# Performance work log

Hardware: AMD Instinct MI355X
Metric: run time of the kernel (lower is better)

## Reference

```python
import jax, jax.numpy as jnp
import numpy as np

B, L, K, H, D = 2, 512, 128, 32, 1024
NUM_EDGES = 2048
SQRT_2PI = 2.5066282746310002
MIN_F32 = float(np.finfo(np.float32).min)
SCALING = K ** -0.5


def setup_inputs() -> dict:
    key = jax.random.key(0)
    ks = jax.random.split(key, 18)
    pos = jax.random.normal(ks[0], (B, L, 3), jnp.float32) * 10.0
    node_type_edge = jax.random.randint(ks[1], (B, L, L, 2), 0, NUM_EDGES)
    adj = jax.random.randint(ks[2], (B, L, L), 0, 2).astype(bool)
    # last 64 tokens of second sample are padding
    padding_mask = jnp.arange(L)[None, :] >= jnp.array([L, L - 64])[:, None]
    molecule_mask = jax.random.randint(ks[3], (B, L), 0, 2).astype(bool)
    clean_mask = jax.random.randint(ks[4], (B, L), 0, 2).astype(bool)
    # parameters
    pos_emb_w = jax.random.normal(ks[5], (K, 3), jnp.float32) * 0.1            # nn.Linear(3, K, bias=False)
    pos_feature_emb_w = jax.random.normal(ks[6], (D, K), jnp.float32) * (K ** -0.5)  # nn.Linear(K, D, bias=False)
    gbf_means = jax.random.uniform(ks[7], (K,), jnp.float32, minval=0.0, maxval=3.0)
    gbf_stds = jax.random.uniform(ks[8], (K,), jnp.float32, minval=0.1, maxval=3.0)
    gbf_mul = jax.random.normal(ks[9], (NUM_EDGES, 1), jnp.float32) * 0.1 + 1.0
    gbf_bias = jax.random.normal(ks[10], (NUM_EDGES, 1), jnp.float32) * 0.1
    proj_w1 = jax.random.normal(ks[11], (K, K), jnp.float32) * (K ** -0.5)     # NonLinear layer1
    proj_b1 = jnp.zeros((K,), jnp.float32)
    proj_w2 = jax.random.normal(ks[12], (H, K), jnp.float32) * (K ** -0.5)     # NonLinear layer2
    proj_b2 = jnp.zeros((H,), jnp.float32)
    pos_proj_w = jax.random.normal(ks[13], (D, K), jnp.float32) * (K ** -0.5)  # pos_embedding_proj
    pos_proj_b = jnp.zeros((D,), jnp.float32)
    return dict(pos=pos, node_type_edge=node_type_edge, adj=adj, padding_mask=padding_mask,
                molecule_mask=molecule_mask, clean_mask=clean_mask,
                pos_emb_w=pos_emb_w, pos_feature_emb_w=pos_feature_emb_w,
                gbf_means=gbf_means, gbf_stds=gbf_stds, gbf_mul=gbf_mul, gbf_bias=gbf_bias,
                proj_w1=proj_w1, proj_b1=proj_b1, proj_w2=proj_w2, proj_b2=proj_b2,
                pos_proj_w=pos_proj_w, pos_proj_b=pos_proj_b)


def reference(pos, node_type_edge, adj, padding_mask, molecule_mask, clean_mask,
              pos_emb_w, pos_feature_emb_w, gbf_means, gbf_stds, gbf_mul, gbf_bias,
              proj_w1, proj_b1, proj_w2, proj_b2, pos_proj_w, pos_proj_b):
    # pairwise distances [B,L,L] (eps-safe sqrt; grad at diagonal is 0)
    delta = pos[:, :, None, :] - pos[:, None, :, :]
    dist0 = jnp.sqrt(jnp.sum(delta * delta, axis=-1) + 1e-12)

    # adj forced True on non-molecule / clean rows
    adj = jnp.where(~molecule_mask[:, :, None], True, adj)
    adj = jnp.where(clean_mask[:, :, None], True, adj)

    # GaussianLayer: per-edge-type affine on dist, then K gaussian kernels -> [B,L,L,K]
    mul = gbf_mul[node_type_edge].sum(axis=-2)    # [B,L,L,1]
    bia = gbf_bias[node_type_edge].sum(axis=-2)   # [B,L,L,1]
    x = mul * dist0[..., None] + bia              # [B,L,L,1]
    std = jnp.abs(gbf_stds) + 1e-5                # [K]
    edge_feature = jnp.exp(-0.5 * jnp.square((x - gbf_means) / std)) / (SQRT_2PI * std)  # [B,L,L,K]

    # NonLinear projection to heads
    h = jax.nn.gelu(jnp.einsum('blmk,jk->blmj', edge_feature, proj_w1) + proj_b1, approximate=False)
    gab = jnp.einsum('blmj,nj->blmn', h, proj_w2) + proj_b2   # [B,L,L,H]

    expand_mask = padding_mask
    gab = jnp.where(expand_mask[:, None, :, None], -jnp.inf, gab)
    gab = jnp.where(~adj[..., None], -jnp.inf, gab)
    gab = jnp.where(padding_mask[:, :, None, None], 0.0, gab)
    graph_attn_bias = jnp.transpose(gab, (0, 3, 1, 2))        # [B,H,L,L]

    dist = graph_attn_bias.sum(axis=1)                        # [B,L,L]
    dist = jnp.where(expand_mask[:, None, :], MIN_F32, dist)
    dist = jnp.where(padding_mask[:, :, None], MIN_F32, dist)

    pos_emb = jnp.einsum('blc,kc->blk', pos, pos_emb_w)       # [B,L,K]
    pos_emb = jnp.where(expand_mask[..., None], 0.0, pos_emb)

    dist = jnp.where(~adj, MIN_F32, dist)
    dist = jax.nn.softmax(dist.astype(jnp.float32) * SCALING, axis=-1)

    pfe = jnp.einsum('blm,bmk->blk', dist, pos_emb)           # weighted aggregation
    pfe = jnp.einsum('blk,dk->bld', pfe, pos_feature_emb_w)   # Linear(K, D, bias=False)

    ef = jnp.where(expand_mask[:, None, :, None], 0.0, edge_feature).sum(axis=-2)  # [B,L,K]
    pfe = pfe + jnp.einsum('blk,dk->bld', ef, pos_proj_w) + pos_proj_b
    pfe = jnp.where(padding_mask[..., None], 0.0, pfe)
    return pfe, graph_attn_bias
```

## Files before the change

### kernel.cpp

```cpp
#include <hip/hip_runtime.h>

typedef __attribute__((ext_vector_type(8))) short short8;
typedef __attribute__((ext_vector_type(4))) float f32x4;

static const int BB = 2;
static const int LL = 512;
#define MIN_F32 (-3.4028234663852886e+38f)
#define NEG_BIG (-1.0e38f)
#define SCALING_F 0.08838834764831845f
#define SQ2PI 2.5066282746310002f

__device__ __forceinline__ float gelu_fast(float x) {
    float s  = x * 0.70710678118654752440f;
    float za = fabsf(s);
    float t  = __builtin_amdgcn_rcpf(fmaf(za, 0.3275911f, 1.0f));
    float p  = t * fmaf(t, fmaf(t, fmaf(t, fmaf(t, 1.061405429f, -1.453152027f),
                                        1.421413741f), -0.284496736f), 0.254829592f);
    float e  = __expf(-za * za);
    float q  = fmaf(-p, e, 1.0f);
    union { float f; unsigned u; } uq, us;
    uq.f = q; us.f = s;
    uq.u = (uq.u & 0x7FFFFFFFu) | (us.u & 0x80000000u);
    float hx = 0.5f * x;
    return fmaf(hx, uq.f, hx);
}
__device__ __forceinline__ unsigned short f2bf(float f) {
    union { float f; unsigned int u; } v; v.f = f;
    unsigned int u = v.u;
    return (unsigned short)((u + 0x7FFFu + ((u >> 16) & 1u)) >> 16);
}
__device__ __forceinline__ int swz(int row, int bytecol) {
    return row * 256 + (bytecol ^ ((row & 7) << 4));
}

__global__ __launch_bounds__(256) void prep_kernel(
    const float* __restrict__ wfe, const float* __restrict__ wp,
    float* __restrict__ wfet, float* __restrict__ wpt)
{
    int idx = blockIdx.x * 256 + threadIdx.x;
    int which = idx >> 17;
    int r = idx & 131071;
    int k = r >> 10;
    int d = r & 1023;
    if (which == 0) wfet[r] = wfe[d * 128 + k];
    else            wpt[r]  = wp[d * 128 + k];
}

__global__ __launch_bounds__(512, 4) void row_kernel(
    const float* __restrict__ pos,
    const int*   __restrict__ nte,
    const unsigned char* __restrict__ adj,
    const unsigned char* __restrict__ padm,
    const unsigned char* __restrict__ molm,
    const unsigned char* __restrict__ clnm,
    const float* __restrict__ gmean,
    const float* __restrict__ gstd,
    const float* __restrict__ gmul,
    const float* __restrict__ gbias,
    const float* __restrict__ w1,
    const float* __restrict__ b1,
    const float* __restrict__ w2,
    const float* __restrict__ b2,
    const float* __restrict__ pw,
    float* __restrict__ out_gab,
    float* __restrict__ pfe1,
    float* __restrict__ efsum)
{
    __shared__ __align__(16) char W1s[128 * 256];
    __shared__ __align__(16) char W2s[32 * 256];
    __shared__ __align__(16) char efs[64 * 256];
    __shared__ __align__(16) char hs [64 * 256];
    __shared__ float dist_row[512];
    __shared__ float xval[512];
    __shared__ unsigned char flgall[512];
    __shared__ float b1s[128];
    __shared__ float b2s[32];
    __shared__ float sred[16];
    __shared__ float dsump[128];

    const int t = threadIdx.x;
    const int row = blockIdx.x;
    const int b = row >> 9;
    const int i = row & 511;

    const int w  = t >> 6;
    const int l  = t & 63;
    const int lr = l & 15;
    const int lq = l >> 4;

    for (int idx = t; idx < 2048 + 512; idx += 512) {
        const float* src; char* dst; int r16, c16;
        if (idx < 2048) { r16 = idx >> 4;          c16 = idx & 15; src = w1 + r16 * 128 + c16 * 8; dst = W1s; }
        else            { r16 = (idx - 2048) >> 4; c16 = (idx - 2048) & 15; src = w2 + r16 * 128 + c16 * 8; dst = W2s; }
        float4 f0 = *(const float4*)(src);
        float4 f1 = *(const float4*)(src + 4);
        uint4 pk;
        pk.x = (unsigned)f2bf(f0.x) | ((unsigned)f2bf(f0.y) << 16);
        pk.y = (unsigned)f2bf(f0.z) | ((unsigned)f2bf(f0.w) << 16);
        pk.z = (unsigned)f2bf(f1.x) | ((unsigned)f2bf(f1.y) << 16);
        pk.w = (unsigned)f2bf(f1.z) | ((unsigned)f2bf(f1.w) << 16);
        *(uint4*)(dst + swz(r16, c16 * 16)) = pk;
    }
    if (t < 128) b1s[t] = b1[t];
    if (t < 32)  b2s[t] = b2[t];

    const bool pad_i = padm[row] != 0;
    const bool force_adj = (clnm[row] != 0) || (molm[row] == 0);
    const float pix = pos[row * 3 + 0], piy = pos[row * 3 + 1], piz = pos[row * 3 + 2];

    {
        int2 e2 = ((const int2*)nte)[row * 512 + t];
        float mul = gmul[e2.x] + gmul[e2.y];
        float bia = gbias[e2.x] + gbias[e2.y];
        float dx = pix - pos[(b * 512 + t) * 3 + 0];
        float dy = piy - pos[(b * 512 + t) * 3 + 1];
        float dz = piz - pos[(b * 512 + t) * 3 + 2];
        float dist = sqrtf(dx * dx + dy * dy + dz * dz + 1e-12f);
        xval[t] = mul * dist + bia;
        int padj = padm[b * 512 + t] ? 1 : 0;
        int adje = (force_adj || adj[row * 512 + t]) ? 2 : 0;
        flgall[t] = (unsigned char)(padj | adje);
    }

    const int kk = t & 127;
    const float gs = fabsf(gstd[kk]) + 1e-5f;
    const float mean_r = gmean[kk];
    const float istd_r = 1.0f / gs;
    const float lnc = -logf(SQ2PI * gs);
    float efacc = 0.f;

    __syncthreads();

    for (int tile = 0; tile < 8; ++tile) {
        const int j0 = tile * 64;
        if (tile > 0 && t < 64) {
            int fl = flgall[j0 - 64 + t];
            bool masked = pad_i || (fl & 1) || !(fl & 2);
            dist_row[j0 - 64 + t] = masked ? MIN_F32 : (dsump[t] + dsump[64 + t]);
        }
        {
            const int jg0 = j0 + (t >> 7) * 16;
            #pragma unroll
            for (int jj = 0; jj < 16; ++jj) {
                int j = jg0 + jj;
                float x = xval[j];
                float mk = (flgall[j] & 1) ? 0.0f : 1.0f;
                float a = (x - mean_r) * istd_r;
                float e = __expf(fmaf(a * a, -0.5f, lnc));
                *(unsigned short*)(efs + swz((j & 63), 2 * kk)) = f2bf(e);
                efacc = fmaf(e, mk, efacc);
            }
        }
        __syncthreads();
        {
            const int jr = (w & 1) * 32;
            const int jc = (w >> 1) * 32;
            f32x4 a00 = {0.f,0.f,0.f,0.f}, a01 = a00, a10 = a00, a11 = a00;
            #pragma unroll
            for (int ks = 0; ks < 4; ++ks) {
                int bcol = ks * 64 + lq * 16;
                short8 av0 = *(const short8*)(efs + swz(jr + lr, bcol));
                short8 av1 = *(const short8*)(efs + swz(jr + 16 + lr, bcol));
                short8 bv0 = *(const short8*)(W1s + swz(jc + lr, bcol));
                short8 bv1 = *(const short8*)(W1s + swz(jc + 16 + lr, bcol));
                a00 = __builtin_amdgcn_mfma_f32_16x16x32_bf16(av0, bv0, a00, 0, 0, 0);
                a01 = __builtin_amdgcn_mfma_f32_16x16x32_bf16(av0, bv1, a01, 0, 0, 0);
                a10 = __builtin_amdgcn_mfma_f32_16x16x32_bf16(av1, bv0, a10, 0, 0, 0);
                a11 = __builtin_amdgcn_mfma_f32_16x16x32_bf16(av1, bv1, a11, 0, 0, 0);
            }
            #pragma unroll
            for (int mi = 0; mi < 2; ++mi) {
                #pragma unroll
                for (int ci = 0; ci < 2; ++ci) {
                    f32x4 acc = (mi == 0) ? (ci == 0 ? a00 : a01) : (ci == 0 ? a10 : a11);
                    int jo = jc + ci * 16 + lr;
                    float bb = b1s[jo];
                    #pragma unroll
                    for (int r = 0; r < 4; ++r) {
                        int j = jr + mi * 16 + lq * 4 + r;
                        *(unsigned short*)(hs + swz(j, 2 * jo)) = f2bf(gelu_fast(acc[r] + bb));
                    }
                }
            }
        }
        __syncthreads();
        {
            const int mt = w >> 2;
            const int jt2 = w & 3;
            f32x4 acc = (f32x4){0.f, 0.f, 0.f, 0.f};
            #pragma unroll
            for (int ks = 0; ks < 4; ++ks) {
                int bcol = ks * 64 + lq * 16;
                short8 av = *(const short8*)(W2s + swz(mt * 16 + lr, bcol));
                short8 bv = *(const short8*)(hs + swz(jt2 * 16 + lr, bcol));
                acc = __builtin_amdgcn_mfma_f32_16x16x32_bf16(av, bv, acc, 0, 0, 0);
            }
            int jl = jt2 * 16 + lr;
            int jg = j0 + jl;
            int fl = flgall[jg];
            bool kill = (fl & 1) || !(fl & 2);
            float dpart = 0.f;
            size_t base = ((size_t)(b * 32 + mt * 16 + lq * 4) * 512 + i) * 512 + jg;
            #pragma unroll
            for (int r = 0; r < 4; ++r) {
                float raw = acc[r] + b2s[mt * 16 + lq * 4 + r];
                dpart += raw;
                float outv = pad_i ? 0.0f : (kill ? NEG_BIG : raw);
                out_gab[base + (size_t)r * 262144] = outv;
            }
            dpart += __shfl_xor(dpart, 16);
            dpart += __shfl_xor(dpart, 32);
            if (l < 16) dsump[mt * 64 + jl] = dpart;
        }
        __syncthreads();
    }

    float* rb = (float*)efs;
    if (t < 64) {
        int fl = flgall[448 + t];
        bool masked = pad_i || (fl & 1) || !(fl & 2);
        dist_row[448 + t] = masked ? MIN_F32 : (dsump[t] + dsump[64 + t]);
    }
    rb[t] = efacc;
    __syncthreads();
    if (t < 128) {
        efsum[(size_t)row * 128 + t] = rb[t] + rb[128 + t] + rb[256 + t] + rb[384 + t];
    }

    float sv = dist_row[t] * SCALING_F;
    float v = sv;
    #pragma unroll
    for (int m = 32; m > 0; m >>= 1) v = fmaxf(v, __shfl_xor(v, m));
    if ((t & 63) == 0) sred[t >> 6] = v;
    __syncthreads();
    float mx = sred[0];
    #pragma unroll
    for (int w8 = 1; w8 < 8; ++w8) mx = fmaxf(mx, sred[w8]);
    float e = expf(sv - mx);
    v = e;
    #pragma unroll
    for (int m = 32; m > 0; m >>= 1) v += __shfl_xor(v, m);
    if ((t & 63) == 0) sred[8 + (t >> 6)] = v;
    __syncthreads();
    float sm = 0.f;
    #pragma unroll
    for (int w8 = 0; w8 < 8; ++w8) sm += sred[8 + w8];
    float p = e / sm;

    float px = pos[(b * 512 + t) * 3 + 0];
    float py = pos[(b * 512 + t) * 3 + 1];
    float pz = pos[(b * 512 + t) * 3 + 2];
    float vx = p * px, vy = p * py, vz = p * pz;
    #pragma unroll
    for (int m = 32; m > 0; m >>= 1) {
        vx += __shfl_xor(vx, m); vy += __shfl_xor(vy, m); vz += __shfl_xor(vz, m);
    }
    __syncthreads();
    if ((t & 63) == 0) {
        int w8 = t >> 6;
        rb[w8] = vx; rb[8 + w8] = vy; rb[16 + w8] = vz;
    }
    __syncthreads();
    if (t < 128) {
        float w0 = 0.f, w1v = 0.f, w2v = 0.f;
        #pragma unroll
        for (int w8 = 0; w8 < 8; ++w8) {
            w0 += rb[w8]; w1v += rb[8 + w8]; w2v += rb[16 + w8];
        }
        pfe1[(size_t)row * 128 + t] = pw[t * 3 + 0] * w0 + pw[t * 3 + 1] * w1v + pw[t * 3 + 2] * w2v;
    }
}

__global__ __launch_bounds__(256) void pfe_kernel(
    const float* __restrict__ pfe1,
    const float* __restrict__ efsum,
    const float* __restrict__ wfet,
    const float* __restrict__ wpt,
    const float* __restrict__ pb,
    const unsigned char* __restrict__ padm,
    float* __restrict__ out)
{
    __shared__ __align__(16) float As[2 * 32 * 132];
    __shared__ __align__(16) float Bs[2 * 16 * 128];
    const int t  = threadIdx.x;
    const int tx = t & 31;
    const int ty = t >> 5;
    const int r0 = (blockIdx.x >> 3) * 32;
    const int d0 = (blockIdx.x & 7) * 128;

    #pragma unroll
    for (int q = 0; q < 16; ++q) {
        int ii = t + q * 256;
        int r = ii >> 7, k = ii & 127;
        As[(0 * 32 + r) * 132 + k] = pfe1 [(size_t)(r0 + r) * 128 + k];
        As[(1 * 32 + r) * 132 + k] = efsum[(size_t)(r0 + r) * 128 + k];
    }

    f32x4 acc[4];
    #pragma unroll
    for (int rr = 0; rr < 4; ++rr) acc[rr] = (f32x4){0.f, 0.f, 0.f, 0.f};

    for (int kc = 0; kc < 8; ++kc) {
        __syncthreads();
        #pragma unroll
        for (int q = 0; q < 2; ++q) {
            int ii = t + q * 256;
            int kr = ii >> 5, dq = ii & 31;
            f32x4 v0 = ((const f32x4*)(wfet + (size_t)(kc * 16 + kr) * 1024 + d0))[dq];
            f32x4 v1 = ((const f32x4*)(wpt  + (size_t)(kc * 16 + kr) * 1024 + d0))[dq];
            *(f32x4*)&Bs[(0 * 16 + kr) * 128 + dq * 4] = v0;
            *(f32x4*)&Bs[(1 * 16 + kr) * 128 + dq * 4] = v1;
        }
        __syncthreads();
        #pragma unroll
        for (int k4 = 0; k4 < 4; ++k4) {
            int kb = kc * 16 + k4 * 4;
            f32x4 a0[4], a1[4];
            #pragma unroll
            for (int rr = 0; rr < 4; ++rr) {
                int r = ty * 4 + rr;
                a0[rr] = *(const f32x4*)&As[(0 * 32 + r) * 132 + kb];
                a1[rr] = *(const f32x4*)&As[(1 * 32 + r) * 132 + kb];
            }
            #pragma unroll
            for (int kq = 0; kq < 4; ++kq) {
                f32x4 b0 = *(const f32x4*)&Bs[(0 * 16 + k4 * 4 + kq) * 128 + tx * 4];
                f32x4 b1 = *(const f32x4*)&Bs[(1 * 16 + k4 * 4 + kq) * 128 + tx * 4];
                #pragma unroll
                for (int rr = 0; rr < 4; ++rr) {
                    acc[rr] += a0[rr][kq] * b0 + a1[rr][kq] * b1;
                }
            }
        }
    }

    f32x4 bv = *(const f32x4*)&pb[d0 + tx * 4];
    #pragma unroll
    for (int rr = 0; rr < 4; ++rr) {
        int row = r0 + ty * 4 + rr;
        f32x4 o = acc[rr] + bv;
        if (padm[row]) o = (f32x4){0.f, 0.f, 0.f, 0.f};
        *(f32x4*)&out[(size_t)row * 1024 + d0 + tx * 4] = o;
    }
}

extern "C" void kernel_launch(void* const* d_in, const int* in_sizes, int n_in,
                              void* d_out, int out_size, void* d_ws, size_t ws_size,
                              hipStream_t stream) {
    const float* pos  = (const float*)d_in[0];
    const int*   nte  = (const int*)d_in[1];
    const unsigned char* adj  = (const unsigned char*)d_in[2];
    const unsigned char* padm = (const unsigned char*)d_in[3];
    const unsigned char* molm = (const unsigned char*)d_in[4];
    const unsigned char* clnm = (const unsigned char*)d_in[5];
    const float* pw    = (const float*)d_in[6];
    const float* wfe   = (const float*)d_in[7];
    const float* gmean = (const float*)d_in[8];
    const float* gstd  = (const float*)d_in[9];
    const float* gmul  = (const float*)d_in[10];
    const float* gbias = (const float*)d_in[11];
    const float* w1    = (const float*)d_in[12];
    const float* b1    = (const float*)d_in[13];
    const float* w2    = (const float*)d_in[14];
    const float* b2    = (const float*)d_in[15];
    const float* wp    = (const float*)d_in[16];
    const float* pb    = (const float*)d_in[17];

    float* out      = (float*)d_out;
    float* out_pfe  = out;
    float* out_gab  = out + (size_t)BB * LL * 1024;

    float* ws    = (float*)d_ws;
    float* pfe1  = ws;
    float* efsum = ws + 131072;
    float* wfet  = ws + 262144;
    float* wpt   = ws + 393216;

    prep_kernel<<<1024, 256, 0, stream>>>(wfe, wp, wfet, wpt);
    row_kernel<<<BB * LL, 512, 0, stream>>>(pos, nte, adj, padm, molm, clnm,
                                            gmean, gstd, gmul, gbias,
                                            w1, b1, w2, b2, pw,
                                            out_gab, pfe1, efsum);
    pfe_kernel<<<256, 256, 0, stream>>>(pfe1, efsum, wfet, wpt, pb, padm, out_pfe);
}
```

Before: 117.3 us.

## Vectorize Gaussian-basis and GELU LDS writes via thread remap and MFMA operand swap

Each thread now computes 8 consecutive Gaussian basis channels for 2 edge positions and writes them to shared memory as one packed 16-byte store, replacing 16 scattered 2-byte stores. The first MFMA now takes the weight as the A operand and the basis tile as the B operand. This transposes the accumulator layout, so GELU outputs go out as packed bf16x2 8-byte stores and the bias comes in as a float4. The per-channel edge-feature sum reduction is reworked to match, now summing 32 partials per channel instead of 4. The cost is more registers held for per-channel constants and accumulators, and a longer final reduction.

```diff
diff --git a/kernel.cpp b/kernel.cpp
--- a/kernel.cpp
+++ b/kernel.cpp
@@ -1,4 +1,5 @@
 #include <hip/hip_runtime.h>
+#include <hip/hip_bf16.h>
 
 typedef __attribute__((ext_vector_type(8))) short short8;
 typedef __attribute__((ext_vector_type(4))) float f32x4;
@@ -23,6 +24,11 @@
     uq.u = (uq.u & 0x7FFFFFFFu) | (us.u & 0x80000000u);
     float hx = 0.5f * x;
     return fmaf(hx, uq.f, hx);
+}
+__device__ __forceinline__ unsigned pack_bf16x2(float lo, float hi) {
+    __hip_bfloat162 h2 = __float22bfloat162_rn(float2{lo, hi});
+    union { __hip_bfloat162 h; unsigned u; } v; v.h = h2;
+    return v.u;
 }
 __device__ __forceinline__ unsigned short f2bf(float f) {
     union { float f; unsigned int u; } v; v.f = f;
@@ -122,12 +128,17 @@
         flgall[t] = (unsigned char)(padj | adje);
     }
 
-    const int kk = t & 127;
-    const float gs = fabsf(gstd[kk]) + 1e-5f;
-    const float mean_r = gmean[kk];
-    const float istd_r = 1.0f / gs;
-    const float lnc = -logf(SQ2PI * gs);
-    float efacc = 0.f;
+    const int k0 = (t & 15) * 8;
+    const int js = t >> 4;
+    float mean_q[8], istd_q[8], lnc_q[8], efacc[8];
+    #pragma unroll
+    for (int q = 0; q < 8; ++q) {
+        float gsv = fabsf(gstd[k0 + q]) + 1e-5f;
+        mean_q[q] = gmean[k0 + q];
+        istd_q[q] = 1.0f / gsv;
+        lnc_q[q]  = -logf(SQ2PI * gsv);
+        efacc[q]  = 0.f;
+    }
 
     __syncthreads();
 
@@ -138,31 +149,36 @@
             bool masked = pad_i || (fl & 1) || !(fl & 2);
             dist_row[j0 - 64 + t] = masked ? MIN_F32 : (dsump[t] + dsump[64 + t]);
         }
-        {
-            const int jg0 = j0 + (t >> 7) * 16;
-            #pragma unroll
-            for (int jj = 0; jj < 16; ++jj) {
-                int j = jg0 + jj;
-                float x = xval[j];
-                float mk = (flgall[j] & 1) ? 0.0f : 1.0f;
-                float a = (x - mean_r) * istd_r;
-                float e = __expf(fmaf(a * a, -0.5f, lnc));
-                *(unsigned short*)(efs + swz((j & 63), 2 * kk)) = f2bf(e);
-                efacc = fmaf(e, mk, efacc);
-            }
+        #pragma unroll
+        for (int jj = 0; jj < 2; ++jj) {
+            int j = js + jj * 32;
+            float x  = xval[j0 + j];
+            float mk = (flgall[j0 + j] & 1) ? 0.0f : 1.0f;
+            unsigned pk[4];
+            #pragma unroll
+            for (int q = 0; q < 4; ++q) {
+                float a0 = (x - mean_q[2*q+0]) * istd_q[2*q+0];
+                float a1 = (x - mean_q[2*q+1]) * istd_q[2*q+1];
+                float e0 = __expf(fmaf(a0 * a0, -0.5f, lnc_q[2*q+0]));
+                float e1 = __expf(fmaf(a1 * a1, -0.5f, lnc_q[2*q+1]));
+                efacc[2*q+0] = fmaf(e0, mk, efacc[2*q+0]);
+                efacc[2*q+1] = fmaf(e1, mk, efacc[2*q+1]);
+                pk[q] = pack_bf16x2(e0, e1);
+            }
+            *(uint4*)(efs + swz(j, 2 * k0)) = make_uint4(pk[0], pk[1], pk[2], pk[3]);
         }
         __syncthreads();
         {
-            const int jr = (w & 1) * 32;
-            const int jc = (w >> 1) * 32;
+            const int jobase = (w & 3) * 32;
+            const int jbase  = (w >> 2) * 32;
             f32x4 a00 = {0.f,0.f,0.f,0.f}, a01 = a00, a10 = a00, a11 = a00;
             #pragma unroll
             for (int ks = 0; ks < 4; ++ks) {
                 int bcol = ks * 64 + lq * 16;
-                short8 av0 = *(const short8*)(efs + swz(jr + lr, bcol));
-                short8 av1 = *(const short8*)(efs + swz(jr + 16 + lr, bcol));
-                short8 bv0 = *(const short8*)(W1s + swz(jc + lr, bcol));
-                short8 bv1 = *(const short8*)(W1s + swz(jc + 16 + lr, bcol));
+                short8 av0 = *(const short8*)(W1s + swz(jobase + lr, bcol));
+                short8 av1 = *(const short8*)(W1s + swz(jobase + 16 + lr, bcol));
+                short8 bv0 = *(const short8*)(efs + swz(jbase + lr, bcol));
+                short8 bv1 = *(const short8*)(efs + swz(jbase + 16 + lr, bcol));
                 a00 = __builtin_amdgcn_mfma_f32_16x16x32_bf16(av0, bv0, a00, 0, 0, 0);
                 a01 = __builtin_amdgcn_mfma_f32_16x16x32_bf16(av0, bv1, a01, 0, 0, 0);
                 a10 = __builtin_amdgcn_mfma_f32_16x16x32_bf16(av1, bv0, a10, 0, 0, 0);
@@ -170,16 +186,18 @@
             }
             #pragma unroll
             for (int mi = 0; mi < 2; ++mi) {
+                int jo0 = jobase + mi * 16 + lq * 4;
+                float4 bb = *(const float4*)&b1s[jo0];
                 #pragma unroll
                 for (int ci = 0; ci < 2; ++ci) {
                     f32x4 acc = (mi == 0) ? (ci == 0 ? a00 : a01) : (ci == 0 ? a10 : a11);
-                    int jo = jc + ci * 16 + lr;
-                    float bb = b1s[jo];
-                    #pragma unroll
-                    for (int r = 0; r < 4; ++r) {
-                        int j = jr + mi * 16 + lq * 4 + r;
-                        *(unsigned short*)(hs + swz(j, 2 * jo)) = f2bf(gelu_fast(acc[r] + bb));
-                    }
+                    int j = jbase + ci * 16 + lr;
+                    float g0 = gelu_fast(acc[0] + bb.x);
+                    float g1 = gelu_fast(acc[1] + bb.y);
+                    float g2 = gelu_fast(acc[2] + bb.z);
+                    float g3 = gelu_fast(acc[3] + bb.w);
+                    uint2 pv = make_uint2(pack_bf16x2(g0, g1), pack_bf16x2(g2, g3));
+                    *(uint2*)(hs + swz(j, 2 * jo0)) = pv;
                 }
             }
         }
@@ -221,10 +239,14 @@
         bool masked = pad_i || (fl & 1) || !(fl & 2);
         dist_row[448 + t] = masked ? MIN_F32 : (dsump[t] + dsump[64 + t]);
     }
-    rb[t] = efacc;
+    *(float4*)&rb[t * 8 + 0] = make_float4(efacc[0], efacc[1], efacc[2], efacc[3]);
+    *(float4*)&rb[t * 8 + 4] = make_float4(efacc[4], efacc[5], efacc[6], efacc[7]);
     __syncthreads();
     if (t < 128) {
-        efsum[(size_t)row * 128 + t] = rb[t] + rb[128 + t] + rb[256 + t] + rb[384 + t];
+        float s = 0.f;
+        #pragma unroll
+        for (int sidx = 0; sidx < 32; ++sidx) s += rb[sidx * 128 + t];
+        efsum[(size_t)row * 128 + t] = s;
     }
 
     float sv = dist_row[t] * SCALING_F;
```

Measured after the change: 115.8 us. No clear change (-1.3%).
